# Kernel optimization log

Measured on AMD Instinct MI355X. Metric: run time of the kernel, lower is better.

The kernel has to match this reference:

```python
import jax, jax.numpy as jnp
import numpy as np

N_NODES = 100000
N_EDGES = 1600000
D_FEAT = 256


def _glorot(key, shape):
    fan_in = shape[0]
    return jax.random.normal(key, shape, jnp.float32) * (1.0 / np.sqrt(fan_in))


def setup_inputs() -> dict:
    key = jax.random.key(0)
    ks = jax.random.split(key, 8)
    return {
        "x": jax.random.normal(ks[0], (N_NODES, D_FEAT), jnp.float32),
        "edge_index": jax.random.randint(ks[1], (2, N_EDGES), 0, N_NODES, jnp.int32),
        "w1": _glorot(ks[2], (D_FEAT, 64)),
        "b1": jnp.zeros((64,), jnp.float32),
        "w2": _glorot(ks[3], (64, 32)),
        "b2": jnp.zeros((32,), jnp.float32),
        "wf1": _glorot(ks[4], (32, 16)),
        "bf1": jnp.zeros((16,), jnp.float32),
        "wf2": _glorot(ks[5], (16, 1)),
        "bf2": jnp.zeros((1,), jnp.float32),
    }


def reference(x, edge_index, w1, b1, w2, b2, wf1, bf1, wf2, bf2):
    n = x.shape[0]
    # GCNConv: add self-loops, symmetric D^{-1/2}(A+I)D^{-1/2} normalization
    loops = jnp.arange(n, dtype=edge_index.dtype)
    src = jnp.concatenate([edge_index[0], loops])  # message sources
    dst = jnp.concatenate([edge_index[1], loops])  # aggregation targets
    deg = jax.ops.segment_sum(jnp.ones_like(dst, x.dtype), dst, num_segments=n)
    dinv = jnp.where(deg > 0, jax.lax.rsqrt(jnp.maximum(deg, 1.0)), 0.0)
    norm = dinv[src] * dinv[dst]  # [E+N]

    def gcn_conv(h, W, b):
        hw = h @ W                                   # dense transform first (smaller msg dim)
        msg = hw[src] * norm[:, None]                # gather + scale
        return jax.ops.segment_sum(msg, dst, num_segments=n) + b  # scatter-add

    h = jax.nn.relu(gcn_conv(x, w1, b1))
    h = jax.nn.relu(gcn_conv(h, w2, b2))
    h = jax.nn.relu(h @ wf1 + bf1)
    out = h @ wf2 + bf2
    return out.squeeze(-1)  # [N]
```

## Files before the change

kernel.cpp:

```cpp
#include <hip/hip_runtime.h>
#include <cstdint>
#include <cstddef>

#define N_NODES 100000
#define N_EDGES 1600000

#define NBK   391
#define NPB   256
#define EPB   ((N_EDGES + NPB - 1) / NPB)
#define NSLOT (NBK * NPB)
#define NSB   ((NSLOT + 1023) / 1024)
#define ES_CAP (N_EDGES + NBK * 2048 + 64)

typedef __attribute__((ext_vector_type(8))) short bf16x8;
typedef __attribute__((ext_vector_type(4))) float f32x4;

__device__ __forceinline__ float b2f(unsigned short u) {
    return __uint_as_float(((unsigned)u) << 16);
}
__device__ __forceinline__ unsigned short f2b(float f) {
    unsigned x = __float_as_uint(f);
    return (unsigned short)((x + 0x7FFFu + ((x >> 16) & 1u)) >> 16);
}

__device__ __forceinline__ void split8(const float4& a0, const float4& a1,
                                       bf16x8& hi, bf16x8& lo) {
    float f[8] = {a0.x, a0.y, a0.z, a0.w, a1.x, a1.y, a1.z, a1.w};
#pragma unroll
    for (int j = 0; j < 8; ++j) {
        unsigned u = __float_as_uint(f[j]);
        hi[j] = (short)(u >> 16);
        float l = f[j] - __uint_as_float(u & 0xFFFF0000u);
        lo[j] = (short)(__float_as_uint(l) >> 16);
    }
}


__global__ __launch_bounds__(256) void k_hist(const int* __restrict__ dst,
                                              int* __restrict__ gcnt, int E) {
    __shared__ int lh[NBK];
    int t = threadIdx.x, bid = blockIdx.x;
    for (int i = t; i < NBK; i += 256) lh[i] = 0;
    __syncthreads();
    int e0 = bid * EPB, e1 = min(E, e0 + EPB);
    for (int e = e0 + t; e < e1; e += 256) atomicAdd(&lh[dst[e] >> 8], 1);
    __syncthreads();
    for (int b = t; b < NBK; b += 256) gcnt[b * NPB + bid] = lh[b];
}

__global__ __launch_bounds__(1024) void k_scanA(int* __restrict__ g,
                                                int* __restrict__ bsum, int ntot) {
    __shared__ int s[1024];
    int t = threadIdx.x;
    int i = blockIdx.x * 1024 + t;
    int v = (i < ntot) ? g[i] : 0;
    s[t] = v;
    __syncthreads();
    for (int o = 1; o < 1024; o <<= 1) {
        int a = (t >= o) ? s[t - o] : 0;
        __syncthreads();
        s[t] += a;
        __syncthreads();
    }
    if (i < ntot) g[i] = s[t] - v;
    if (t == 1023) bsum[blockIdx.x] = s[1023];
}

__global__ __launch_bounds__(128) void k_scanB(int* __restrict__ bsum, int nb) {
    __shared__ int s[128];
    int t = threadIdx.x;
    int v = (t < nb) ? bsum[t] : 0;
    s[t] = v;
    __syncthreads();
    for (int o = 1; o < 128; o <<= 1) {
        int a = (t >= o) ? s[t - o] : 0;
        __syncthreads();
        s[t] += a;
        __syncthreads();
    }
    if (t < nb) bsum[t] = s[t] - v;
}

__global__ __launch_bounds__(1024) void k_scanC(int* __restrict__ g,
                                                const int* __restrict__ bsum, int ntot) {
    int i = blockIdx.x * 1024 + threadIdx.x;
    if (i < ntot) g[i] += bsum[blockIdx.x];
}

__global__ __launch_bounds__(256) void k_partition(const int* __restrict__ src,
                                                   const int* __restrict__ dst,
                                                   const int* __restrict__ base,
                                                   unsigned* __restrict__ ebuf, int E) {
    __shared__ int lcur[NBK];
    int t = threadIdx.x, bid = blockIdx.x;
    for (int b = t; b < NBK; b += 256) lcur[b] = base[b * NPB + bid];
    __syncthreads();
    int e0 = bid * EPB, e1 = min(E, e0 + EPB);
    for (int e = e0 + t; e < e1; e += 256) {
        int d = dst[e];
        int b = d >> 8;
        int p = atomicAdd(&lcur[b], 1);
        ebuf[p] = (unsigned)src[e] | ((unsigned)(d & 255) << 20);
    }
}

__global__ __launch_bounds__(256) void k_bucket_csr(const int* __restrict__ base,
                                                    const unsigned* __restrict__ ebuf,
                                                    int* __restrict__ cnt,
                                                    float* __restrict__ dinv,
                                                    int* __restrict__ off,
                                                    int* __restrict__ es, int n) {
    __shared__ int lc[256];
    __shared__ int ss[256];
    __shared__ int lo[256];
    __shared__ int lcur[256];
    int b = blockIdx.x, t = threadIdx.x;
    int rstart = base[b * NPB];
    int rend = (b == NBK - 1) ? N_EDGES : base[(b + 1) * NPB];
    int wstart = ((rstart + 7) & ~7) + b * 2048;
    lc[t] = 0;
    __syncthreads();
    for (int e = rstart + t; e < rend; e += 256) atomicAdd(&lc[(int)(ebuf[e] >> 20)], 1);
    __syncthreads();
    int v = lc[t];
    int vp = (v + 7) & ~7;
    ss[t] = vp;
    __syncthreads();
    for (int o = 1; o < 256; o <<= 1) {
        int a = (t >= o) ? ss[t - o] : 0;
        __syncthreads();
        ss[t] += a;
        __syncthreads();
    }
    lo[t] = ss[t] - vp;
    lcur[t] = 0;
    int node = b * 256 + t;
    if (node < n) {
        cnt[node] = vp;
        dinv[node] = rsqrtf((float)v + 1.0f);
        off[node] = wstart + lo[t];
    }
    __syncthreads();
    for (int e = rstart + t; e < rend; e += 256) {
        unsigned u = ebuf[e];
        int l = (int)(u >> 20);
        int p = atomicAdd(&lcur[l], 1);
        es[wstart + lo[l] + p] = (int)(u & 0xFFFFFu);
    }
    for (int q = v; q < vp; ++q) es[wstart + lo[t] + q] = N_NODES;
}

__global__ void k_zero_sent(unsigned short* __restrict__ hwb1,
                            unsigned short* __restrict__ hwb2) {
    int t = threadIdx.x;
    if (t < 64) hwb1[(size_t)N_NODES * 64 + t] = 0;
    else hwb2[(size_t)N_NODES * 32 + (t - 64)] = 0;
}


__global__ __launch_bounds__(256) void k_gemm1_mfma(const float* __restrict__ x,
                                                    const float* __restrict__ w,
                                                    const float* __restrict__ dinv,
                                                    unsigned short* __restrict__ out, int M) {
    __shared__ unsigned short Bhi[32 * 64 * 8];
    __shared__ unsigned short Blo[32 * 64 * 8];
    int t = threadIdx.x;
    int wave = t >> 6, lane = t & 63;

    {
        int c = t & 63;
        int kg0 = t >> 6;
#pragma unroll
        for (int i = 0; i < 8; ++i) {
            int kgrp = kg0 + i * 4;
            bf16x8 h8, l8;
#pragma unroll
            for (int j = 0; j < 8; ++j) {
                float f = w[(size_t)(kgrp * 8 + j) * 64 + c];
                unsigned u = __float_as_uint(f);
                h8[j] = (short)(u >> 16);
                float l = f - __uint_as_float(u & 0xFFFF0000u);
                l8[j] = (short)(__float_as_uint(l) >> 16);
            }
            *(bf16x8*)&Bhi[(kgrp * 64 + c) * 8] = h8;
            *(bf16x8*)&Blo[(kgrp * 64 + c) * 8] = l8;
        }
    }
    __syncthreads();

    int row0w = blockIdx.x * 64 + wave * 16;
    int r = row0w + (lane & 15); if (r >= M) r = M - 1;
    const float* xr = x + (size_t)r * 256 + (lane >> 4) * 8;

    f32x4 acc[4] = {{0.f,0.f,0.f,0.f},{0.f,0.f,0.f,0.f},{0.f,0.f,0.f,0.f},{0.f,0.f,0.f,0.f}};

#pragma unroll
    for (int kf = 0; kf < 8; ++kf) {
        float4 a0 = *(const float4*)(xr + kf * 32);
        float4 a1 = *(const float4*)(xr + kf * 32 + 4);
        bf16x8 ahi, alo;
        split8(a0, a1, ahi, alo);
        int kgrpR = kf * 4 + (lane >> 4);
#pragma unroll
        for (int cf = 0; cf < 4; ++cf) {
            bf16x8 bhi = *(const bf16x8*)&Bhi[(kgrpR * 64 + cf * 16 + (lane & 15)) * 8];
            bf16x8 blo = *(const bf16x8*)&Blo[(kgrpR * 64 + cf * 16 + (lane & 15)) * 8];
            acc[cf] = __builtin_amdgcn_mfma_f32_16x16x32_bf16(ahi, bhi, acc[cf], 0, 0, 0);
            acc[cf] = __builtin_amdgcn_mfma_f32_16x16x32_bf16(ahi, blo, acc[cf], 0, 0, 0);
            acc[cf] = __builtin_amdgcn_mfma_f32_16x16x32_bf16(alo, bhi, acc[cf], 0, 0, 0);
        }
    }

#pragma unroll
    for (int j = 0; j < 4; ++j) {
        int rr = row0w + (lane >> 4) * 4 + j;
        if (rr < M) {
            float s = dinv[rr];
#pragma unroll
            for (int cf = 0; cf < 4; ++cf)
                out[(size_t)rr * 64 + cf * 16 + (lane & 15)] = f2b(acc[cf][j] * s);
        }
    }
}


__global__ __launch_bounds__(256) void k_gemm2_mfma(const float* __restrict__ h,
                                                    const float* __restrict__ w,
                                                    const float* __restrict__ dinv,
                                                    unsigned short* __restrict__ out, int M) {
    __shared__ unsigned short Bhi[8 * 32 * 8];
    __shared__ unsigned short Blo[8 * 32 * 8];
    int t = threadIdx.x;
    int wave = t >> 6, lane = t & 63;

    {
        int c = t & 31;
        int kg = t >> 5;
        bf16x8 h8, l8;
#pragma unroll
        for (int j = 0; j < 8; ++j) {
            float f = w[(size_t)(kg * 8 + j) * 32 + c];
            unsigned u = __float_as_uint(f);
            h8[j] = (short)(u >> 16);
            float l = f - __uint_as_float(u & 0xFFFF0000u);
            l8[j] = (short)(__float_as_uint(l) >> 16);
        }
        *(bf16x8*)&Bhi[(kg * 32 + c) * 8] = h8;
        *(bf16x8*)&Blo[(kg * 32 + c) * 8] = l8;
    }
    __syncthreads();

    int row0w = blockIdx.x * 64 + wave * 16;
    int r = row0w + (lane & 15); if (r >= M) r = M - 1;
    const float* xr = h + (size_t)r * 64 + (lane >> 4) * 8;

    f32x4 acc[2] = {{0.f,0.f,0.f,0.f},{0.f,0.f,0.f,0.f}};

#pragma unroll
    for (int kf = 0; kf < 2; ++kf) {
        float4 a0 = *(const float4*)(xr + kf * 32);
        float4 a1 = *(const float4*)(xr + kf * 32 + 4);
        bf16x8 ahi, alo;
        split8(a0, a1, ahi, alo);
        int kgrpR = kf * 4 + (lane >> 4);
#pragma unroll
        for (int cf = 0; cf < 2; ++cf) {
            bf16x8 bhi = *(const bf16x8*)&Bhi[(kgrpR * 32 + cf * 16 + (lane & 15)) * 8];
            bf16x8 blo = *(const bf16x8*)&Blo[(kgrpR * 32 + cf * 16 + (lane & 15)) * 8];
            acc[cf] = __builtin_amdgcn_mfma_f32_16x16x32_bf16(ahi, bhi, acc[cf], 0, 0, 0);
            acc[cf] = __builtin_amdgcn_mfma_f32_16x16x32_bf16(ahi, blo, acc[cf], 0, 0, 0);
            acc[cf] = __builtin_amdgcn_mfma_f32_16x16x32_bf16(alo, bhi, acc[cf], 0, 0, 0);
        }
    }

#pragma unroll
    for (int j = 0; j < 4; ++j) {
        int rr = row0w + (lane >> 4) * 4 + j;
        if (rr < M) {
            float s = dinv[rr];
#pragma unroll
            for (int cf = 0; cf < 2; ++cf)
                out[(size_t)rr * 32 + cf * 16 + (lane & 15)] = f2b(acc[cf][j] * s);
        }
    }
}


__global__ __launch_bounds__(256) void k_agg1(const unsigned short* __restrict__ hwb,
                                              const float* __restrict__ dinv,
                                              const int* __restrict__ cnt,
                                              const int* __restrict__ off,
                                              const int* __restrict__ es,
                                              const float* __restrict__ bias,
                                              float* __restrict__ hout) {
    int t = blockIdx.x * 256 + threadIdx.x;
    int node = t >> 6;
    int c = t & 63;
    float dn = dinv[node];
    float acc0 = b2f(hwb[(size_t)node * 64 + c]);
    float acc1 = 0.0f;
    const int* ep = es + off[node];
    int mp = cnt[node];
    for (int j = 0; j < mp; j += 8) {
        int4 e0 = *(const int4*)&ep[j];
        int4 e1 = *(const int4*)&ep[j + 4];
        float v0 = b2f(hwb[(size_t)e0.x * 64 + c]);
        float v1 = b2f(hwb[(size_t)e0.y * 64 + c]);
        float v2 = b2f(hwb[(size_t)e0.z * 64 + c]);
        float v3 = b2f(hwb[(size_t)e0.w * 64 + c]);
        float v4 = b2f(hwb[(size_t)e1.x * 64 + c]);
        float v5 = b2f(hwb[(size_t)e1.y * 64 + c]);
        float v6 = b2f(hwb[(size_t)e1.z * 64 + c]);
        float v7 = b2f(hwb[(size_t)e1.w * 64 + c]);
        acc0 += (v0 + v1) + (v2 + v3);
        acc1 += (v4 + v5) + (v6 + v7);
    }
    float acc = acc0 + acc1;
    hout[(size_t)node * 64 + c] = fmaxf(fmaf(dn, acc, bias[c]), 0.0f);
}


__global__ __launch_bounds__(256) void k_agg2_mlp(const unsigned short* __restrict__ hwb,
                                                  const float* __restrict__ dinv,
                                                  const int* __restrict__ cnt,
                                                  const int* __restrict__ off,
                                                  const int* __restrict__ es,
                                                  const float* __restrict__ bias2,
                                                  const float* __restrict__ wf1,
                                                  const float* __restrict__ bf1,
                                                  const float* __restrict__ wf2,
                                                  const float* __restrict__ bf2,
                                                  float* __restrict__ out) {
    __shared__ float hs[8][33];
    __shared__ float W1[512];
    __shared__ float B1[16];
    __shared__ float W2[16];
    int t = threadIdx.x;
    W1[t] = wf1[t];
    W1[t + 256] = wf1[t + 256];
    if (t < 16) { B1[t] = bf1[t]; W2[t] = wf2[t]; }

    int node0 = blockIdx.x * 8;
    int nl = t >> 5;
    int c = t & 31;
    int node = node0 + nl;
    float dn = dinv[node];
    float acc0 = b2f(hwb[(size_t)node * 32 + c]);
    float acc1 = 0.0f;
    const int* ep = es + off[node];
    int mp = cnt[node];
    for (int j = 0; j < mp; j += 8) {
        int4 e0 = *(const int4*)&ep[j];
        int4 e1 = *(const int4*)&ep[j + 4];
        float v0 = b2f(hwb[(size_t)e0.x * 32 + c]);
        float v1 = b2f(hwb[(size_t)e0.y * 32 + c]);
        float v2 = b2f(hwb[(size_t)e0.z * 32 + c]);
        float v3 = b2f(hwb[(size_t)e0.w * 32 + c]);
        float v4 = b2f(hwb[(size_t)e1.x * 32 + c]);
        float v5 = b2f(hwb[(size_t)e1.y * 32 + c]);
        float v6 = b2f(hwb[(size_t)e1.z * 32 + c]);
        float v7 = b2f(hwb[(size_t)e1.w * 32 + c]);
        acc0 += (v0 + v1) + (v2 + v3);
        acc1 += (v4 + v5) + (v6 + v7);
    }
    hs[nl][c] = fmaxf(fmaf(dn, acc0 + acc1, bias2[c]), 0.0f);
    __syncthreads();
    if (t < 128) {
        int nn = t >> 4, jj = t & 15;
        float s = B1[jj];
#pragma unroll
        for (int k = 0; k < 32; ++k) s += hs[nn][k] * W1[k * 16 + jj];
        float p = fmaxf(s, 0.0f) * W2[jj];
        p += __shfl_xor(p, 1);
        p += __shfl_xor(p, 2);
        p += __shfl_xor(p, 4);
        p += __shfl_xor(p, 8);
        if (jj == 0) out[node0 + nn] = p + bf2[0];
    }
}


extern "C" void kernel_launch(void* const* d_in, const int* in_sizes, int n_in,
                              void* d_out, int out_size, void* d_ws, size_t ws_size,
                              hipStream_t stream) {
    const float* x   = (const float*)d_in[0];
    const int*   ei  = (const int*)d_in[1];
    const float* w1  = (const float*)d_in[2];
    const float* b1  = (const float*)d_in[3];
    const float* w2  = (const float*)d_in[4];
    const float* b2  = (const float*)d_in[5];
    const float* wf1 = (const float*)d_in[6];
    const float* bf1 = (const float*)d_in[7];
    const float* wf2 = (const float*)d_in[8];
    const float* bf2 = (const float*)d_in[9];

    const int n = N_NODES;
    const int E = N_EDGES;
    const int* srcp = ei;
    const int* dstp = ei + E;

    char* p = (char*)d_ws;
    auto take = [&](size_t bytes) {
        char* r = p;
        p += (bytes + 255) & ~(size_t)255;
        return r;
    };
    float* dinv = (float*)take((size_t)n * 4);
    int*   cnt  = (int*)take((size_t)n * 4);
    int*   off  = (int*)take((size_t)n * 4);
    int*   gcnt = (int*)take((size_t)NSLOT * 4);
    int*   bsum = (int*)take(512);
    int*   es   = (int*)take((size_t)ES_CAP * 4);
    unsigned short* hwb1 = (unsigned short*)take((size_t)(n + 1) * 64 * 2);
    unsigned short* hwb2 = (unsigned short*)take((size_t)(n + 1) * 32 * 2);
    float* h1   = (float*)take((size_t)n * 64 * 4);
    unsigned* ebuf = (unsigned*)hwb1;

    k_zero_sent<<<1, 96, 0, stream>>>(hwb1, hwb2);
    k_hist<<<NPB, 256, 0, stream>>>(dstp, gcnt, E);
    k_scanA<<<NSB, 1024, 0, stream>>>(gcnt, bsum, NSLOT);
    k_scanB<<<1, 128, 0, stream>>>(bsum, NSB);
    k_scanC<<<NSB, 1024, 0, stream>>>(gcnt, bsum, NSLOT);
    k_partition<<<NPB, 256, 0, stream>>>(srcp, dstp, gcnt, ebuf, E);
    k_bucket_csr<<<NBK, 256, 0, stream>>>(gcnt, ebuf, cnt, dinv, off, es, n);

    k_gemm1_mfma<<<(n + 63) / 64, 256, 0, stream>>>(x, w1, dinv, hwb1, n);
    k_agg1<<<(n * 64) / 256, 256, 0, stream>>>(hwb1, dinv, cnt, off, es, b1, h1);
    k_gemm2_mfma<<<(n + 63) / 64, 256, 0, stream>>>(h1, w2, dinv, hwb2, n);
    k_agg2_mlp<<<n / 8, 256, 0, stream>>>(hwb2, dinv, cnt, off, es, b2,
                                          wf1, bf1, wf2, bf2, (float*)d_out);
}
```

Before: 178.8 us.

## Fuse layer-1 aggregation with layer-2 GEMM and drop small launch kernels

Merges the first GCN aggregation with the second dense transform, so aggregated rows go through LDS into an MFMA split-bf16 GEMM instead of round-tripping a 100k×64 fp32 buffer through global memory. The sentinel zeroing moves into the histogram kernel, and the separate block-sum scan kernel is removed by having each scanC block reduce the preceding block sums itself. This cuts about 51 MB of intermediate traffic and three launches. In exchange, each aggregation block now idles half its waves during the GEMM phase and reloads W2 from global memory per block.

Measured after the change: 164.2 us. -8.2%, faster.

```diff
diff --git a/kernel.cpp b/kernel.cpp
--- a/kernel.cpp
+++ b/kernel.cpp
@@ -23,9 +23,7 @@
     return (unsigned short)((x + 0x7FFFu + ((x >> 16) & 1u)) >> 16);
 }
 
-__device__ __forceinline__ void split8(const float4& a0, const float4& a1,
-                                       bf16x8& hi, bf16x8& lo) {
-    float f[8] = {a0.x, a0.y, a0.z, a0.w, a1.x, a1.y, a1.z, a1.w};
+__device__ __forceinline__ void split8a(const float* f, bf16x8& hi, bf16x8& lo) {
 #pragma unroll
     for (int j = 0; j < 8; ++j) {
         unsigned u = __float_as_uint(f[j]);
@@ -34,12 +32,23 @@
         lo[j] = (short)(__float_as_uint(l) >> 16);
     }
 }
+__device__ __forceinline__ void split8(const float4& a0, const float4& a1,
+                                       bf16x8& hi, bf16x8& lo) {
+    float f[8] = {a0.x, a0.y, a0.z, a0.w, a1.x, a1.y, a1.z, a1.w};
+    split8a(f, hi, lo);
+}
 
 
 __global__ __launch_bounds__(256) void k_hist(const int* __restrict__ dst,
-                                              int* __restrict__ gcnt, int E) {
+                                              int* __restrict__ gcnt,
+                                              unsigned short* __restrict__ hwb1,
+                                              unsigned short* __restrict__ hwb2, int E) {
     __shared__ int lh[NBK];
     int t = threadIdx.x, bid = blockIdx.x;
+    if (bid == 0) {
+        if (t < 64) hwb1[(size_t)N_NODES * 64 + t] = 0;
+        else if (t < 96) hwb2[(size_t)N_NODES * 32 + (t - 64)] = 0;
+    }
     for (int i = t; i < NBK; i += 256) lh[i] = 0;
     __syncthreads();
     int e0 = bid * EPB, e1 = min(E, e0 + EPB);
@@ -66,25 +75,19 @@
     if (t == 1023) bsum[blockIdx.x] = s[1023];
 }
 
-__global__ __launch_bounds__(128) void k_scanB(int* __restrict__ bsum, int nb) {
-    __shared__ int s[128];
-    int t = threadIdx.x;
-    int v = (t < nb) ? bsum[t] : 0;
-    s[t] = v;
-    __syncthreads();
-    for (int o = 1; o < 128; o <<= 1) {
-        int a = (t >= o) ? s[t - o] : 0;
-        __syncthreads();
-        s[t] += a;
-        __syncthreads();
-    }
-    if (t < nb) bsum[t] = s[t] - v;
-}
-
 __global__ __launch_bounds__(1024) void k_scanC(int* __restrict__ g,
                                                 const int* __restrict__ bsum, int ntot) {
-    int i = blockIdx.x * 1024 + threadIdx.x;
-    if (i < ntot) g[i] += bsum[blockIdx.x];
+    __shared__ int sp[1024];
+    int t = threadIdx.x;
+    sp[t] = (t < blockIdx.x && t < NSB) ? bsum[t] : 0;
+    __syncthreads();
+    for (int o = 512; o > 0; o >>= 1) {
+        if (t < o) sp[t] += sp[t + o];
+        __syncthreads();
+    }
+    int pref = sp[0];
+    int i = blockIdx.x * 1024 + t;
+    if (i < ntot) g[i] += pref;
 }
 
 __global__ __launch_bounds__(256) void k_partition(const int* __restrict__ src,
@@ -150,13 +153,6 @@
     for (int q = v; q < vp; ++q) es[wstart + lo[t] + q] = N_NODES;
 }
 
-__global__ void k_zero_sent(unsigned short* __restrict__ hwb1,
-                            unsigned short* __restrict__ hwb2) {
-    int t = threadIdx.x;
-    if (t < 64) hwb1[(size_t)N_NODES * 64 + t] = 0;
-    else hwb2[(size_t)N_NODES * 32 + (t - 64)] = 0;
-}
-
 
 __global__ __launch_bounds__(256) void k_gemm1_mfma(const float* __restrict__ x,
                                                     const float* __restrict__ w,
@@ -224,99 +220,74 @@
 }
 
 
-__global__ __launch_bounds__(256) void k_gemm2_mfma(const float* __restrict__ h,
-                                                    const float* __restrict__ w,
+__global__ __launch_bounds__(256) void k_agg1_gemm2(const unsigned short* __restrict__ hwb,
                                                     const float* __restrict__ dinv,
-                                                    unsigned short* __restrict__ out, int M) {
-    __shared__ unsigned short Bhi[8 * 32 * 8];
-    __shared__ unsigned short Blo[8 * 32 * 8];
-    int t = threadIdx.x;
-    int wave = t >> 6, lane = t & 63;
-
-    {
-        int c = t & 31;
-        int kg = t >> 5;
-        bf16x8 h8, l8;
-#pragma unroll
-        for (int j = 0; j < 8; ++j) {
-            float f = w[(size_t)(kg * 8 + j) * 32 + c];
-            unsigned u = __float_as_uint(f);
-            h8[j] = (short)(u >> 16);
-            float l = f - __uint_as_float(u & 0xFFFF0000u);
-            l8[j] = (short)(__float_as_uint(l) >> 16);
-        }
-        *(bf16x8*)&Bhi[(kg * 32 + c) * 8] = h8;
-        *(bf16x8*)&Blo[(kg * 32 + c) * 8] = l8;
-    }
-    __syncthreads();
-
-    int row0w = blockIdx.x * 64 + wave * 16;
-    int r = row0w + (lane & 15); if (r >= M) r = M - 1;
-    const float* xr = h + (size_t)r * 64 + (lane >> 4) * 8;
-
-    f32x4 acc[2] = {{0.f,0.f,0.f,0.f},{0.f,0.f,0.f,0.f}};
-
-#pragma unroll
-    for (int kf = 0; kf < 2; ++kf) {
-        float4 a0 = *(const float4*)(xr + kf * 32);
-        float4 a1 = *(const float4*)(xr + kf * 32 + 4);
-        bf16x8 ahi, alo;
-        split8(a0, a1, ahi, alo);
-        int kgrpR = kf * 4 + (lane >> 4);
-#pragma unroll
-        for (int cf = 0; cf < 2; ++cf) {
-            bf16x8 bhi = *(const bf16x8*)&Bhi[(kgrpR * 32 + cf * 16 + (lane & 15)) * 8];
-            bf16x8 blo = *(const bf16x8*)&Blo[(kgrpR * 32 + cf * 16 + (lane & 15)) * 8];
-            acc[cf] = __builtin_amdgcn_mfma_f32_16x16x32_bf16(ahi, bhi, acc[cf], 0, 0, 0);
-            acc[cf] = __builtin_amdgcn_mfma_f32_16x16x32_bf16(ahi, blo, acc[cf], 0, 0, 0);
-            acc[cf] = __builtin_amdgcn_mfma_f32_16x16x32_bf16(alo, bhi, acc[cf], 0, 0, 0);
-        }
-    }
-
-#pragma unroll
-    for (int j = 0; j < 4; ++j) {
-        int rr = row0w + (lane >> 4) * 4 + j;
-        if (rr < M) {
-            float s = dinv[rr];
-#pragma unroll
-            for (int cf = 0; cf < 2; ++cf)
-                out[(size_t)rr * 32 + cf * 16 + (lane & 15)] = f2b(acc[cf][j] * s);
-        }
-    }
-}
-
-
-__global__ __launch_bounds__(256) void k_agg1(const unsigned short* __restrict__ hwb,
-                                              const float* __restrict__ dinv,
-                                              const int* __restrict__ cnt,
-                                              const int* __restrict__ off,
-                                              const int* __restrict__ es,
-                                              const float* __restrict__ bias,
-                                              float* __restrict__ hout) {
-    int t = blockIdx.x * 256 + threadIdx.x;
-    int node = t >> 6;
-    int c = t & 63;
-    float dn = dinv[node];
-    float acc0 = b2f(hwb[(size_t)node * 64 + c]);
-    float acc1 = 0.0f;
-    const int* ep = es + off[node];
-    int mp = cnt[node];
-    for (int j = 0; j < mp; j += 8) {
-        int4 e0 = *(const int4*)&ep[j];
-        int4 e1 = *(const int4*)&ep[j + 4];
-        float v0 = b2f(hwb[(size_t)e0.x * 64 + c]);
-        float v1 = b2f(hwb[(size_t)e0.y * 64 + c]);
-        float v2 = b2f(hwb[(size_t)e0.z * 64 + c]);
-        float v3 = b2f(hwb[(size_t)e0.w * 64 + c]);
-        float v4 = b2f(hwb[(size_t)e1.x * 64 + c]);
-        float v5 = b2f(hwb[(size_t)e1.y * 64 + c]);
-        float v6 = b2f(hwb[(size_t)e1.z * 64 + c]);
-        float v7 = b2f(hwb[(size_t)e1.w * 64 + c]);
-        acc0 += (v0 + v1) + (v2 + v3);
-        acc1 += (v4 + v5) + (v6 + v7);
-    }
-    float acc = acc0 + acc1;
-    hout[(size_t)node * 64 + c] = fmaxf(fmaf(dn, acc, bias[c]), 0.0f);
+                                                    const int* __restrict__ cnt,
+                                                    const int* __restrict__ off,
+                                                    const int* __restrict__ es,
+                                                    const float* __restrict__ bias,
+                                                    const float* __restrict__ w2,
+                                                    unsigned short* __restrict__ out) {
+    __shared__ float hs[16][68];
+    int t = threadIdx.x;
+    int wv = t >> 6, lane = t & 63;
+    int node0 = blockIdx.x * 16;
+    float bl = bias[lane];
+
+#pragma unroll
+    for (int i = 0; i < 4; ++i) {
+        int node = node0 + wv * 4 + i;
+        float dn = dinv[node];
+        float acc0 = b2f(hwb[(size_t)node * 64 + lane]);
+        float acc1 = 0.0f;
+        const int* ep = es + off[node];
+        int mp = cnt[node];
+        for (int j = 0; j < mp; j += 8) {
+            int4 e0 = *(const int4*)&ep[j];
+            int4 e1 = *(const int4*)&ep[j + 4];
+            float v0 = b2f(hwb[(size_t)e0.x * 64 + lane]);
+            float v1 = b2f(hwb[(size_t)e0.y * 64 + lane]);
+            float v2 = b2f(hwb[(size_t)e0.z * 64 + lane]);
+            float v3 = b2f(hwb[(size_t)e0.w * 64 + lane]);
+            float v4 = b2f(hwb[(size_t)e1.x * 64 + lane]);
+            float v5 = b2f(hwb[(size_t)e1.y * 64 + lane]);
+            float v6 = b2f(hwb[(size_t)e1.z * 64 + lane]);
+            float v7 = b2f(hwb[(size_t)e1.w * 64 + lane]);
+            acc0 += (v0 + v1) + (v2 + v3);
+            acc1 += (v4 + v5) + (v6 + v7);
+        }
+        hs[wv * 4 + i][lane] = fmaxf(fmaf(dn, acc0 + acc1, bl), 0.0f);
+    }
+    __syncthreads();
+
+    if (wv < 2) {
+        int colbase = wv * 16;
+        int r = lane & 15;
+        int kg = lane >> 4;
+        f32x4 acc = {0.f, 0.f, 0.f, 0.f};
+#pragma unroll
+        for (int ks = 0; ks < 2; ++ks) {
+            float a[8], b[8];
+#pragma unroll
+            for (int j = 0; j < 8; ++j) {
+                int k = ks * 32 + kg * 8 + j;
+                a[j] = hs[r][k];
+                b[j] = w2[(size_t)k * 32 + colbase + r];
+            }
+            bf16x8 ahi, alo, bhi, blo;
+            split8a(a, ahi, alo);
+            split8a(b, bhi, blo);
+            acc = __builtin_amdgcn_mfma_f32_16x16x32_bf16(ahi, bhi, acc, 0, 0, 0);
+            acc = __builtin_amdgcn_mfma_f32_16x16x32_bf16(ahi, blo, acc, 0, 0, 0);
+            acc = __builtin_amdgcn_mfma_f32_16x16x32_bf16(alo, bhi, acc, 0, 0, 0);
+        }
+#pragma unroll
+        for (int reg = 0; reg < 4; ++reg) {
+            int row = kg * 4 + reg;
+            int nd = node0 + row;
+            out[(size_t)nd * 32 + colbase + r] = f2b(acc[reg] * dinv[nd]);
+        }
+    }
 }
 
 
@@ -413,20 +384,16 @@
     int*   es   = (int*)take((size_t)ES_CAP * 4);
     unsigned short* hwb1 = (unsigned short*)take((size_t)(n + 1) * 64 * 2);
     unsigned short* hwb2 = (unsigned short*)take((size_t)(n + 1) * 32 * 2);
-    float* h1   = (float*)take((size_t)n * 64 * 4);
     unsigned* ebuf = (unsigned*)hwb1;
 
-    k_zero_sent<<<1, 96, 0, stream>>>(hwb1, hwb2);
-    k_hist<<<NPB, 256, 0, stream>>>(dstp, gcnt, E);
+    k_hist<<<NPB, 256, 0, stream>>>(dstp, gcnt, hwb1, hwb2, E);
     k_scanA<<<NSB, 1024, 0, stream>>>(gcnt, bsum, NSLOT);
-    k_scanB<<<1, 128, 0, stream>>>(bsum, NSB);
     k_scanC<<<NSB, 1024, 0, stream>>>(gcnt, bsum, NSLOT);
     k_partition<<<NPB, 256, 0, stream>>>(srcp, dstp, gcnt, ebuf, E);
     k_bucket_csr<<<NBK, 256, 0, stream>>>(gcnt, ebuf, cnt, dinv, off, es, n);
 
     k_gemm1_mfma<<<(n + 63) / 64, 256, 0, stream>>>(x, w1, dinv, hwb1, n);
-    k_agg1<<<(n * 64) / 256, 256, 0, stream>>>(hwb1, dinv, cnt, off, es, b1, h1);
-    k_gemm2_mfma<<<(n + 63) / 64, 256, 0, stream>>>(h1, w2, dinv, hwb2, n);
+    k_agg1_gemm2<<<n / 16, 256, 0, stream>>>(hwb1, dinv, cnt, off, es, b1, w2, hwb2);
     k_agg2_mlp<<<n / 8, 256, 0, stream>>>(hwb2, dinv, cnt, off, es, b2,
                                           wf1, bf1, wf2, bf2, (float*)d_out);
 }
```
